# Kernel tuning notes

Measured on AMD Instinct MI355X. Metric: run time of the kernel, lower is better.

## Reference

```python
import jax, jax.numpy as jnp
import numpy as np

QLEN, MLEN, BSZ, DM, NH, DH, DI = 512, 512, 8, 1024, 16, 64, 4096
KLEN = QLEN + MLEN
EPS = 1e-5
NEG = -1e30


def layer_norm(x, g, b):
    mu = jnp.mean(x, axis=-1, keepdims=True)
    var = jnp.mean(jnp.square(x - mu), axis=-1, keepdims=True)
    return (x - mu) * jax.lax.rsqrt(var + EPS) * g + b


def rel_shift(x):
    # x: [qlen, rlen, bsz, n_head] -> Transformer-XL relative shift
    q, r, b, n = x.shape
    zp = jnp.zeros((q, 1, b, n), x.dtype)
    xp = jnp.concatenate([zp, x], axis=1).reshape(r + 1, q, b, n)
    return xp[1:].reshape(q, r, b, n)


def setup_inputs() -> dict:
    key = jax.random.key(0)
    ks = jax.random.split(key, 12)
    inp = {
        "w": jax.random.normal(ks[0], (QLEN, BSZ, DM), jnp.float32),
        "r": jax.random.normal(ks[1], (KLEN, DM), jnp.float32),
        "mems": jax.random.normal(ks[2], (MLEN, BSZ, DM), jnp.float32),
        "w_qkv": jax.random.normal(ks[3], (DM, 3 * NH * DH), jnp.float32) * 0.02,
        "w_r": jax.random.normal(ks[4], (DM, NH * DH), jnp.float32) * 0.02,
        "w_o": jax.random.normal(ks[5], (NH * DH, DM), jnp.float32) * 0.02,
        "r_w_bias": jax.random.normal(ks[6], (NH, DH), jnp.float32) * 0.02,
        "r_r_bias": jax.random.normal(ks[7], (NH, DH), jnp.float32) * 0.02,
        "ln1_g": jnp.ones((DM,), jnp.float32),
        "ln1_b": jnp.zeros((DM,), jnp.float32),
        "ff_w1": jax.random.normal(ks[8], (DM, DI), jnp.float32) * 0.02,
        "ff_b1": jnp.zeros((DI,), jnp.float32),
        "ff_w2": jax.random.normal(ks[9], (DI, DM), jnp.float32) * 0.02,
        "ff_b2": jnp.zeros((DM,), jnp.float32),
        "ln2_g": jnp.ones((DM,), jnp.float32),
        "ln2_b": jnp.zeros((DM,), jnp.float32),
    }
    # causal mask with memory: query i (global pos MLEN+i) cannot attend to j > MLEN+i
    i = jnp.arange(QLEN)[:, None]
    j = jnp.arange(KLEN)[None, :]
    inp["attn_mask"] = j > (i + MLEN)
    return inp


def reference(w, r, mems, attn_mask, w_qkv, w_r, w_o, r_w_bias, r_r_bias,
              ln1_g, ln1_b, ff_w1, ff_b1, ff_w2, ff_b2, ln2_g, ln2_b):
    qlen, bsz = w.shape[0], w.shape[1]
    scale = 1.0 / (DH ** 0.5)
    cat = jnp.concatenate([mems, w], axis=0)                 # [klen, b, d]
    klen = cat.shape[0]
    heads = cat @ w_qkv                                      # [klen, b, 3*H*D]
    hq, hk, hv = jnp.split(heads, 3, axis=-1)
    hq = hq[-qlen:].reshape(qlen, bsz, NH, DH)
    hk = hk.reshape(klen, bsz, NH, DH)
    hv = hv.reshape(klen, bsz, NH, DH)
    r_head_k = (r @ w_r).reshape(klen, NH, DH)               # [rlen, H, D]

    AC = jnp.einsum('ibnd,jbnd->ijbn', hq + r_w_bias, hk)
    BD = rel_shift(jnp.einsum('ibnd,jnd->ijbn', hq + r_r_bias, r_head_k))
    score = (AC + BD) * scale                                # [q, k, b, h]
    score = jnp.where(attn_mask[:, :, None, None], NEG, score)
    prob = jax.nn.softmax(score, axis=1)
    vec = jnp.einsum('ijbn,jbnd->ibnd', prob, hv).reshape(qlen, bsz, NH * DH)
    attn_out = vec @ w_o
    h = layer_norm(w + attn_out, ln1_g, ln1_b)               # post-LN
    ff = jax.nn.relu(h @ ff_w1 + ff_b1) @ ff_w2 + ff_b2
    return layer_norm(h + ff, ln2_g, ln2_b)
```

## Files before the change

### kernel.cpp

```cpp
#include <hip/hip_runtime.h>
#include <hip/hip_bf16.h>

#define QLEN 512
#define MLEN 512
#define KLEN 1024
#define BSZ 8
#define DM 1024
#define NH 16
#define DH 64
#define DI 4096
#define NEGF (-1e30f)
#define HM_PART ((size_t)8388608)

typedef unsigned short u16;
typedef __attribute__((ext_vector_type(8))) short short8;
typedef __attribute__((ext_vector_type(4))) short s16x4;
typedef __attribute__((ext_vector_type(4))) float f32x4;

__device__ __forceinline__ float bf2f(u16 u) {
    union { unsigned i; float f; } x; x.i = ((unsigned)u) << 16; return x.f;
}
__device__ __forceinline__ u16 f2bf(float f) {
    __hip_bfloat16 h = __float2bfloat16(f);
    return *reinterpret_cast<u16*>(&h);
}
__device__ __forceinline__ float4 ldg4(const float* p) {
    return *reinterpret_cast<const float4*>(p);
}
__device__ __forceinline__ void gload16(const void* g, void* l) {
    __builtin_amdgcn_global_load_lds(
        (const __attribute__((address_space(1))) void*)g,
        (__attribute__((address_space(3))) void*)l, 16, 0, 0);
}

__global__ __launch_bounds__(256) void cast_all(
    const float* __restrict__ mems, const float* __restrict__ w,
    const float* __restrict__ r, u16* __restrict__ catB, u16* __restrict__ rB)
{
    int idx = (blockIdx.x * 256 + threadIdx.x) * 4;
    const float* src;
    u16* dst;
    if (idx < 8388608) {
        src = (idx < 4194304) ? (mems + idx) : (w + idx - 4194304);
        dst = catB + idx;
    } else {
        int i2 = idx - 8388608;
        if (i2 >= 1048576) return;
        src = r + i2;
        dst = rB + i2;
    }
    float4 v = ldg4(src);
    u16 o[4] = { f2bf(v.x), f2bf(v.y), f2bf(v.z), f2bf(v.w) };
    *reinterpret_cast<uint2*>(dst) = *reinterpret_cast<uint2*>(o);
}

__device__ __forceinline__ void tr32(
    const float* __restrict__ W, u16* __restrict__ WT, int K, int N, int k0, int n0)
{
    __shared__ float tile[32][33];
    const int tx = threadIdx.x & 31, ty = threadIdx.x >> 5;
    #pragma unroll
    for (int j = 0; j < 4; ++j)
        tile[ty + j * 8][tx] = W[(size_t)(k0 + ty + j * 8) * N + n0 + tx];
    __syncthreads();
    #pragma unroll
    for (int j = 0; j < 4; ++j)
        WT[(size_t)(n0 + ty + j * 8) * K + k0 + tx] = f2bf(tile[tx][ty + j * 8]);
}

__global__ __launch_bounds__(256) void transpose_all(
    const float* __restrict__ w_qkv, u16* __restrict__ qkvT,
    const float* __restrict__ w_r,   u16* __restrict__ wrT,
    const float* __restrict__ w_o,   u16* __restrict__ woT,
    const float* __restrict__ ffw1,  u16* __restrict__ f1T,
    const float* __restrict__ ffw2,  u16* __restrict__ f2T)
{
    int id = blockIdx.x;
    if (id < 3072)       { int l = id;        tr32(w_qkv, qkvT, 1024, 3072, (l / 96) * 32, (l % 96) * 32); }
    else if (id < 4096)  { int l = id - 3072; tr32(w_r,   wrT,  1024, 1024, (l / 32) * 32, (l % 32) * 32); }
    else if (id < 5120)  { int l = id - 4096; tr32(w_o,   woT,  1024, 1024, (l / 32) * 32, (l % 32) * 32); }
    else if (id < 9216)  { int l = id - 5120; tr32(ffw1,  f1T,  1024, 4096, (l / 128) * 32, (l % 128) * 32); }
    else                 { int l = id - 9216; tr32(ffw2,  f2T,  4096, 1024, (l / 32) * 32, (l % 32) * 32); }
}

__global__ __launch_bounds__(256) void v_transpose(
    const u16* __restrict__ Vhm, u16* __restrict__ Vg)
{
    const int bn = blockIdx.x;
    const int kt = blockIdx.y;
    const int t = threadIdx.x;
    __shared__ u16 L[64 * 64];

    #pragma unroll
    for (int rep = 0; rep < 2; ++rep) {
        int idx = t + rep * 256;
        int key = idx >> 3, dc = (idx & 7) * 8;
        short8 v = *reinterpret_cast<const short8*>(
            &Vhm[((size_t)bn * 1024 + kt * 64 + key) * 64 + dc]);
        *reinterpret_cast<short8*>((char*)L + key * 128 + ((dc * 2) ^ ((key & 7) << 4))) = v;
    }
    __syncthreads();
    #pragma unroll
    for (int rep = 0; rep < 2; ++rep) {
        int idx = t + rep * 256;
        int d = idx >> 3, kc = (idx & 7) * 8;
        short8 o;
        #pragma unroll
        for (int e = 0; e < 8; ++e)
            o[e] = *(const short*)((char*)L + (kc + e) * 128 + ((d * 2) ^ (((kc + e) & 7) << 4)));
        *reinterpret_cast<short8*>(&Vg[((size_t)(bn * 64 + d)) * KLEN + kt * 64 + kc]) = o;
    }
}

template<bool BIAS, bool RELU, int OUT>
__global__ __launch_bounds__(256) void gemm_mfma(
    const u16* __restrict__ A, const u16* __restrict__ BT,
    const float* __restrict__ bias,
    float* __restrict__ Cf, u16* __restrict__ Cb,
    int M, int N, int K, int lda, int ldb)
{
    __shared__ u16 As[128 * 64];
    __shared__ u16 Bs[128 * 64];
    const int bm = blockIdx.y * 128, bn = blockIdx.x * 128;
    const int z = blockIdx.z;
    A  += (size_t)z * K;
    BT += (size_t)z * K;
    const size_t zoff = (size_t)z * M * N;
    const int t = threadIdx.x;
    const int w = t >> 6, l = t & 63, lg = l >> 4, lq = l & 15;
    const int wm = (w >> 1) * 64, wn = (w & 1) * 64;
    const int r8 = l >> 3, slot = l & 7;
    const int gcol = (slot * 16) ^ (r8 << 4);

    f32x4 acc[4][4];
    #pragma unroll
    for (int x = 0; x < 4; ++x)
        #pragma unroll
        for (int y = 0; y < 4; ++y)
            acc[x][y] = (f32x4){0.f, 0.f, 0.f, 0.f};

    const int swzr = (lq & 7) << 4;

    for (int k0 = 0; k0 < K; k0 += 64) {
        __syncthreads();
        #pragma unroll
        for (int it = 0; it < 4; ++it) {
            const int base_row = w * 8 + it * 32;
            gload16((const char*)A + (((size_t)(bm + base_row + r8) * lda + k0) << 1) + gcol,
                    (char*)As + base_row * 128);
            gload16((const char*)BT + (((size_t)(bn + base_row + r8) * ldb + k0) << 1) + gcol,
                    (char*)Bs + base_row * 128);
        }
        __syncthreads();
        #pragma unroll
        for (int ks = 0; ks < 2; ++ks) {
            const int cb = (ks * 64 + 16 * lg) ^ swzr;
            short8 af[4], bf_[4];
            #pragma unroll
            for (int x = 0; x < 4; ++x)
                af[x] = *reinterpret_cast<const short8*>((char*)As + (wm + 16 * x + lq) * 128 + cb);
            #pragma unroll
            for (int y = 0; y < 4; ++y)
                bf_[y] = *reinterpret_cast<const short8*>((char*)Bs + (wn + 16 * y + lq) * 128 + cb);
            #pragma unroll
            for (int x = 0; x < 4; ++x)
                #pragma unroll
                for (int y = 0; y < 4; ++y)
                    acc[x][y] = __builtin_amdgcn_mfma_f32_16x16x32_bf16(af[x], bf_[y], acc[x][y], 0, 0, 0);
        }
    }
    const int nn = ((bn + wn) >> 6) & 15;
    #pragma unroll
    for (int x = 0; x < 4; ++x) {
        #pragma unroll
        for (int y = 0; y < 4; ++y) {
            const int col = bn + wn + 16 * y + lq;
            #pragma unroll
            for (int r = 0; r < 4; ++r) {
                const int row = bm + wm + 16 * x + 4 * lg + r;
                float v = acc[x][y][r];
                if constexpr (BIAS) { if (z == 0) v += bias[col]; }
                if constexpr (RELU) v = fmaxf(v, 0.f);
                if constexpr (OUT == 0) Cf[zoff + (size_t)row * N + col] = v;
                else if constexpr (OUT == 1) Cb[zoff + (size_t)row * N + col] = f2bf(v);
                else
                    Cb[((size_t)nn * 1024 + row) * 64 + 16 * y + lq] = f2bf(v);
            }
        }
    }
}

template<bool BIAS, bool RELU, int OUT>
__global__ __launch_bounds__(512, 2) void gemm_deep(
    const u16* __restrict__ A, const u16* __restrict__ BT,
    const float* __restrict__ bias,
    float* __restrict__ Cf, u16* __restrict__ Cb,
    int M, int N, int K, int lda, int ldb)
{
    __shared__ u16 lds[3 * 24576];
    const int bm = blockIdx.y * 256, bn = blockIdx.x * 128;
    const int z = blockIdx.z;
    A  += (size_t)z * K;
    BT += (size_t)z * K;
    const size_t zoff = (size_t)z * M * N;
    const int t = threadIdx.x;
    const int w = t >> 6, l = t & 63, lg = l >> 4, lq = l & 15;
    const int wm = (w >> 1) * 64;
    const int wn = (w & 1) * 64;
    const int srow = t >> 3, slot = t & 7;
    const int gcol = (slot * 16) ^ ((srow & 7) << 4);
    const int swzr = (lq & 7) << 4;

    auto stage_tile = [&](int kt, int buf) {
        const int k0 = kt * 64;
        char* Ab = (char*)lds + buf * 49152 + w * 1024;
        char* Bb = (char*)lds + buf * 49152 + 32768 + w * 1024;
        #pragma unroll
        for (int i = 0; i < 4; ++i)
            gload16((const char*)A + (((size_t)(bm + i * 64 + srow) * lda + k0) << 1) + gcol,
                    Ab + i * 8192);
        #pragma unroll
        for (int i = 0; i < 2; ++i)
            gload16((const char*)BT + (((size_t)(bn + i * 64 + srow) * ldb + k0) << 1) + gcol,
                    Bb + i * 8192);
    };

    f32x4 acc[4][4];
    #pragma unroll
    for (int x = 0; x < 4; ++x)
        #pragma unroll
        for (int y = 0; y < 4; ++y)
            acc[x][y] = (f32x4){0.f, 0.f, 0.f, 0.f};

    const int NT = K >> 6;
    stage_tile(0, 0);
    stage_tile(1, 1);

    for (int kt = 0; kt < NT; ++kt) {
        if (kt < NT - 1) asm volatile("s_waitcnt vmcnt(6)" ::: "memory");
        else             asm volatile("s_waitcnt vmcnt(0)" ::: "memory");
        __builtin_amdgcn_s_barrier();
        __builtin_amdgcn_sched_barrier(0);
        if (kt + 2 < NT) stage_tile(kt + 2, (kt + 2) % 3);

        const char* Ab = (const char*)lds + (kt % 3) * 49152;
        const char* Bb = Ab + 32768;
        #pragma unroll
        for (int ks = 0; ks < 2; ++ks) {
            const int cb = (ks * 64 + 16 * lg) ^ swzr;
            short8 af[4], bf_[4];
            #pragma unroll
            for (int x = 0; x < 4; ++x)
                af[x] = *reinterpret_cast<const short8*>(Ab + (wm + 16 * x + lq) * 128 + cb);
            #pragma unroll
            for (int y = 0; y < 4; ++y)
                bf_[y] = *reinterpret_cast<const short8*>(Bb + (wn + 16 * y + lq) * 128 + cb);
            __builtin_amdgcn_s_setprio(1);
            #pragma unroll
            for (int x = 0; x < 4; ++x)
                #pragma unroll
                for (int y = 0; y < 4; ++y)
                    acc[x][y] = __builtin_amdgcn_mfma_f32_16x16x32_bf16(af[x], bf_[y], acc[x][y], 0, 0, 0);
            __builtin_amdgcn_s_setprio(0);
        }
    }

    #pragma unroll
    for (int x = 0; x < 4; ++x) {
        #pragma unroll
        for (int y = 0; y < 4; ++y) {
            const int col = bn + wn + 16 * y + lq;
            #pragma unroll
            for (int r = 0; r < 4; ++r) {
                const int row = bm + wm + 16 * x + 4 * lg + r;
                float v = acc[x][y][r];
                if constexpr (BIAS) { if (z == 0) v += bias[col]; }
                if constexpr (RELU) v = fmaxf(v, 0.f);
                if constexpr (OUT == 0) Cf[zoff + (size_t)row * N + col] = v;
                else Cb[zoff + (size_t)row * N + col] = f2bf(v);
            }
        }
    }
}

template<bool BIAS, bool RELU, int OUT>
__global__ __launch_bounds__(512, 2) void gemm256(
    const u16* __restrict__ A, const u16* __restrict__ BT,
    const float* __restrict__ bias, u16* __restrict__ Cb,
    int N, int K, int lda, int ldb, int nbx)
{
    __shared__ u16 lds[2 * 32768];
    int bm, bn;
    if constexpr (OUT == 2) {
        const int id = blockIdx.x;
        if (id < 64) { bm = 4096 + (id >> 2) * 256; bn = (id & 3) * 256; }
        else         { int j = id - 64; bm = (j >> 3) * 256; bn = 1024 + (j & 7) * 256; }
    } else {
        bm = (blockIdx.x / nbx) * 256; bn = (blockIdx.x % nbx) * 256;
    }
    const int t = threadIdx.x;
    const int w = t >> 6, l = t & 63, lg = l >> 4, lq = l & 15;
    const int wm = (w >> 2) * 128;
    const int wn = (w & 3) * 64;
    const int srow = t >> 3, slot = t & 7;
    const int gcol = (slot * 16) ^ ((srow & 7) << 4);
    const int swzr = (lq & 7) << 4;

    auto stage_unit = [&](int kt, char* buf, int u) {
        const int k0 = kt * 64;
        if (u < 2) {
            #pragma unroll
            for (int i = 0; i < 2; ++i) {
                int g = u * 2 + i;
                gload16((const char*)BT + (((size_t)(bn + g * 64 + srow) * ldb + k0) << 1) + gcol,
                        buf + 32768 + g * 8192 + w * 1024);
            }
        } else {
            #pragma unroll
            for (int i = 0; i < 2; ++i) {
                int g = (u - 2) + i * 2;
                gload16((const char*)A + (((size_t)(bm + g * 64 + srow) * lda + k0) << 1) + gcol,
                        buf + g * 8192 + w * 1024);
            }
        }
    };

    f32x4 acc[8][4];
    #pragma unroll
    for (int m = 0; m < 8; ++m)
        #pragma unroll
        for (int y = 0; y < 4; ++y)
            acc[m][y] = (f32x4){0.f, 0.f, 0.f, 0.f};

    const int NT = K >> 6;
    #pragma unroll
    for (int u = 0; u < 4; ++u) stage_unit(0, (char*)lds, u);

    for (int kt = 0; kt < NT; ++kt) {
        const char* Ab = (const char*)lds + (kt & 1) * 65536;
        const char* Bb = Ab + 32768;
        char* nbuf = (char*)lds + ((kt + 1) & 1) * 65536;
        const bool pf = (kt + 1 < NT);

        short8 bf_[4];
        #pragma unroll
        for (int ks = 0; ks < 2; ++ks) {
            const int cb = (ks * 64 + 16 * lg) ^ swzr;
            #pragma unroll
            for (int mh = 0; mh < 2; ++mh) {
                const int ph = ks * 2 + mh;
                if (ph == 0) {
                    asm volatile("s_waitcnt vmcnt(2)" ::: "memory");
                } else if (ph == 1) {
                    if (pf) asm volatile("s_waitcnt vmcnt(2)" ::: "memory");
                    else    asm volatile("s_waitcnt vmcnt(0)" ::: "memory");
                }
                __builtin_amdgcn_s_barrier();
                short8 af[4];
                if (mh == 0) {
                    #pragma unroll
                    for (int y = 0; y < 4; ++y)
                        bf_[y] = *reinterpret_cast<const short8*>(Bb + (wn + 16 * y + lq) * 128 + cb);
                }
                #pragma unroll
                for (int x = 0; x < 4; ++x)
                    af[x] = *reinterpret_cast<const short8*>(
                        Ab + (wm + mh * 64 + 16 * x + lq) * 128 + cb);
                if (pf) stage_unit(kt + 1, nbuf, ph);
                asm volatile("s_waitcnt lgkmcnt(0)" ::: "memory");
                __builtin_amdgcn_sched_barrier(0);
                __builtin_amdgcn_s_setprio(1);
                #pragma unroll
                for (int x = 0; x < 4; ++x)
                    #pragma unroll
                    for (int y = 0; y < 4; ++y)
                        acc[mh * 4 + x][y] = __builtin_amdgcn_mfma_f32_16x16x32_bf16(
                            af[x], bf_[y], acc[mh * 4 + x][y], 0, 0, 0);
                __builtin_amdgcn_s_setprio(0);
            }
        }
    }

    #pragma unroll
    for (int m = 0; m < 8; ++m) {
        #pragma unroll
        for (int y = 0; y < 4; ++y) {
            const int col = bn + wn + 16 * y + lq;
            #pragma unroll
            for (int r = 0; r < 4; ++r) {
                const int row = bm + wm + m * 16 + 4 * lg + r;
                float v = acc[m][y][r];
                if constexpr (BIAS) v += bias[col];
                if constexpr (RELU) v = fmaxf(v, 0.f);
                if constexpr (OUT == 2) {
                    const int part = col >> 10, nn = (col >> 6) & 15;
                    Cb[(size_t)part * HM_PART
                       + ((size_t)((row & 7) * 16 + nn) * 1024 + (row >> 3)) * 64
                       + (col & 63)] = f2bf(v);
                } else {
                    Cb[(size_t)row * N + col] = f2bf(v);
                }
            }
        }
    }
}

__global__ __launch_bounds__(512, 4) void attn_mfma(
    const u16* __restrict__ Hm,
    const u16* __restrict__ Vg,
    const u16* __restrict__ rhm,
    const float* __restrict__ rwb, const float* __restrict__ rrb,
    u16* __restrict__ vec)
{
    const int bnidx = blockIdx.x;
    const int b = bnidx >> 4;
    const int n = bnidx & 15;
    const int i0 = (3 - blockIdx.y) * 128;
    const int t = threadIdx.x;
    const int w = t >> 6;
    const int l = t & 63;
    const int lg = l >> 4, lq = l & 15;
    const int r8 = l >> 3, sl = l & 7;

    const u16* Qh = Hm;
    const u16* Kh = Hm + HM_PART;

    __shared__ u16 Ks[64 * 64];
    __shared__ u16 Vt[64 * 64];
    __shared__ u16 Rs[192 * 64];
    __shared__ u16 SbO[8 * 16 * 84];
    __shared__ u16 Ps[8 * 16 * 64];

    u16* SbW = SbO + w * 16 * 84;
    u16* PsW = Ps + w * 16 * 64;
    const int swzr = (lq & 7) << 4;
    const int stg_swz = (sl * 16) ^ (r8 << 4);

    short8 qw[2], qr[2];
    {
        const size_t qbase = ((size_t)bnidx * 1024 + MLEN + i0 + 16 * w + lq) * 64;
        #pragma unroll
        for (int ks = 0; ks < 2; ++ks) {
            short8 qv = *reinterpret_cast<const short8*>(&Qh[qbase + ks * 32 + 8 * lg]);
            short8 xw, xr;
            #pragma unroll
            for (int e = 0; e < 8; ++e) {
                float f = bf2f((u16)qv[e]);
                int d = ks * 32 + 8 * lg + e;
                xw[e] = (short)f2bf(f + rwb[n * 64 + d]);
                xr[e] = (short)f2bf(f + rrb[n * 64 + d]);
            }
            qw[ks] = xw; qr[ks] = xr;
        }
    }

    float m_run = NEGF, l_run = 0.f;
    f32x4 acc[4];
    #pragma unroll
    for (int df = 0; df < 4; ++df) acc[df] = (f32x4){0.f, 0.f, 0.f, 0.f};

    const int s0 = 112 - 16 * w;
    const int rbase = 384 - i0;
    const int ntiles = i0 / 64 + 10;

    for (int tile = 0; tile < ntiles; ++tile) {
        const int j0 = tile << 6;
        __syncthreads();
        gload16((const char*)Kh + (((size_t)bnidx * 1024 + j0 + w * 8 + r8) * 64 << 1) + stg_swz,
                (char*)Ks + w * 1024);
        gload16((const char*)Vg + ((((size_t)bnidx * 64 + w * 8 + r8) * KLEN + j0) << 1) + stg_swz,
                (char*)Vt + w * 1024);
        if (tile == 0) {
            #pragma unroll
            for (int pass = 0; pass < 3; ++pass) {
                int row = pass * 64 + w * 8 + r8;
                int o = rbase + row;
                o = o > (KLEN - 1) ? (KLEN - 1) : o;
                gload16((const char*)rhm + (((size_t)n * 1024 + o) * 64 << 1) + stg_swz,
                        (char*)Rs + pass * 8192 + w * 1024);
            }
        } else {
            const int g = tile + 2;
            int o = rbase + g * 64 + w * 8 + r8;
            o = o > (KLEN - 1) ? (KLEN - 1) : o;
            gload16((const char*)rhm + (((size_t)n * 1024 + o) * 64 << 1) + stg_swz,
                    (char*)Rs + (g % 3) * 8192 + w * 1024);
        }
        __syncthreads();

        const int bmax = i0 + 16 * w + 15 + MLEN - j0;
        if (bmax < 0) continue;

        __builtin_amdgcn_s_setprio(1);
        #pragma unroll
        for (int ff = 0; ff < 5; ++ff) {
            const int olf = s0 + 16 * ff;
            const int srowb = ((tile + (olf >> 6)) % 3) * 64 + (olf & 63);
            f32x4 d = (f32x4){0.f, 0.f, 0.f, 0.f};
            #pragma unroll
            for (int ks = 0; ks < 2; ++ks) {
                short8 a = *reinterpret_cast<const short8*>(
                    (char*)Rs + (srowb + lq) * 128 + ((ks * 64 + 16 * lg) ^ swzr));
                d = __builtin_amdgcn_mfma_f32_16x16x32_bf16(a, qr[ks], d, 0, 0, 0);
            }
            s16x4 pk;
            #pragma unroll
            for (int r = 0; r < 4; ++r) pk[r] = (short)f2bf(d[r]);
            *reinterpret_cast<s16x4*>(&SbW[lq * 84 + 16 * ff + 4 * lg]) = pk;
        }
        f32x4 dac[4];
        #pragma unroll
        for (int f = 0; f < 4; ++f) {
            f32x4 d = (f32x4){0.f, 0.f, 0.f, 0.f};
            #pragma unroll
            for (int ks = 0; ks < 2; ++ks) {
                short8 a = *reinterpret_cast<const short8*>(
                    (char*)Ks + (16 * f + lq) * 128 + ((ks * 64 + 16 * lg) ^ swzr));
                d = __builtin_amdgcn_mfma_f32_16x16x32_bf16(a, qw[ks], d, 0, 0, 0);
            }
            dac[f] = d;
        }
        __builtin_amdgcn_s_setprio(0);

        const bool fullTile = (i0 + 16 * w + MLEN - j0) >= 63;
        float sv[4][4];
        float mx = NEGF;
        if (fullTile) {
            #pragma unroll
            for (int f = 0; f < 4; ++f)
                #pragma unroll
                for (int r = 0; r < 4; ++r) {
                    int k = 16 * f + 4 * lg + r;
                    float bd = bf2f(SbW[lq * 84 + k - lq + 15]);
                    float x = (dac[f][r] + bd) * 0.125f;
                    sv[f][r] = x;
                    mx = fmaxf(mx, x);
                }
        } else {
            const int bound = i0 + 16 * w + lq + MLEN - j0;
            #pragma unroll
            for (int f = 0; f < 4; ++f)
                #pragma unroll
                for (int r = 0; r < 4; ++r) {
                    int k = 16 * f + 4 * lg + r;
                    float bd = bf2f(SbW[lq * 84 + k - lq + 15]);
                    float x = (k <= bound) ? (dac[f][r] + bd) * 0.125f : NEGF;
                    sv[f][r] = x;
                    mx = fmaxf(mx, x);
                }
        }
        mx = fmaxf(mx, __shfl_xor(mx, 16));
        mx = fmaxf(mx, __shfl_xor(mx, 32));
        const bool defer = (__all(mx <= m_run + 8.0f) != 0);
        const float m_new = defer ? m_run : fmaxf(m_run, mx);
        float ps = 0.f;
        #pragma unroll
        for (int f = 0; f < 4; ++f) {
            s16x4 pk;
            #pragma unroll
            for (int r = 0; r < 4; ++r) {
                float p = __expf(sv[f][r] - m_new);
                ps += p;
                pk[r] = (short)f2bf(p);
            }
            *reinterpret_cast<s16x4*>(
                (char*)PsW + lq * 128 + (((4 * f + lg) ^ ((lq & 7) << 1)) << 3)) = pk;
        }
        ps += __shfl_xor(ps, 16);
        ps += __shfl_xor(ps, 32);
        if (defer) {
            l_run += ps;
        } else {
            float alpha = __expf(m_run - m_new);
            l_run = l_run * alpha + ps;
            m_run = m_new;
            float alr[4];
            #pragma unroll
            for (int r = 0; r < 4; ++r) alr[r] = __shfl(alpha, 20 * lg + r);
            #pragma unroll
            for (int df = 0; df < 4; ++df)
                #pragma unroll
                for (int r = 0; r < 4; ++r) acc[df][r] *= alr[r];
        }

        __builtin_amdgcn_s_setprio(1);
        #pragma unroll
        for (int df = 0; df < 4; ++df) {
            f32x4 a = acc[df];
            #pragma unroll
            for (int ks = 0; ks < 2; ++ks) {
                short8 pa = *reinterpret_cast<const short8*>(
                    (char*)PsW + lq * 128 + ((ks * 64 + 16 * lg) ^ swzr));
                short8 vb = *reinterpret_cast<const short8*>(
                    (char*)Vt + (16 * df + lq) * 128 + ((ks * 64 + 16 * lg) ^ swzr));
                a = __builtin_amdgcn_mfma_f32_16x16x32_bf16(pa, vb, a, 0, 0, 0);
            }
            acc[df] = a;
        }
        __builtin_amdgcn_s_setprio(0);
    }

    float inv[4];
    #pragma unroll
    for (int r = 0; r < 4; ++r) inv[r] = 1.f / __shfl(l_run, 20 * lg + r);
    #pragma unroll
    for (int df = 0; df < 4; ++df) {
        #pragma unroll
        for (int r = 0; r < 4; ++r) {
            const int il = 16 * w + 4 * lg + r;
            float o = acc[df][r] * inv[r];
            vec[((size_t)((i0 + il) * BSZ + b)) * DM + n * 64 + 16 * df + lq] = f2bf(o);
        }
    }
}

template<int NRES, bool WB>
__global__ __launch_bounds__(256) void ln_res_kernel(
    const float* __restrict__ x, const float* __restrict__ res,
    const float* __restrict__ res2,
    const float* __restrict__ g, const float* __restrict__ bta,
    float* __restrict__ out, u16* __restrict__ outb)
{
    const int row = blockIdx.x;
    const int t = threadIdx.x;
    const int lane = t & 63, wv = t >> 6;
    __shared__ float red0[4], red1[4];

    float4 a = ldg4(&x[(size_t)row * DM + t * 4]);
    float4 b = ldg4(&res[(size_t)row * DM + t * 4]);
    float v0 = a.x + b.x, v1 = a.y + b.y, v2 = a.z + b.z, v3 = a.w + b.w;
    if constexpr (NRES == 2) {
        float4 c = ldg4(&res2[(size_t)row * DM + t * 4]);
        v0 += c.x; v1 += c.y; v2 += c.z; v3 += c.w;
    }
    float s = v0 + v1 + v2 + v3;
    #pragma unroll
    for (int o = 32; o; o >>= 1) s += __shfl_xor(s, o);
    if (lane == 0) red0[wv] = s;
    __syncthreads();
    float mu = (red0[0] + red0[1] + red0[2] + red0[3]) * (1.f / DM);
    float d0 = v0 - mu, d1 = v1 - mu, d2 = v2 - mu, d3 = v3 - mu;
    float q = d0*d0 + d1*d1 + d2*d2 + d3*d3;
    #pragma unroll
    for (int o = 32; o; o >>= 1) q += __shfl_xor(q, o);
    if (lane == 0) red1[wv] = q;
    __syncthreads();
    float var = (red1[0] + red1[1] + red1[2] + red1[3]) * (1.f / DM);
    float rs = rsqrtf(var + 1e-5f);
    float4 gv = ldg4(&g[t * 4]);
    float4 bv = ldg4(&bta[t * 4]);
    float o0 = d0 * rs * gv.x + bv.x;
    float o1 = d1 * rs * gv.y + bv.y;
    float o2 = d2 * rs * gv.z + bv.z;
    float o3 = d3 * rs * gv.w + bv.w;
    float4 o4 = make_float4(o0, o1, o2, o3);
    *reinterpret_cast<float4*>(&out[(size_t)row * DM + t * 4]) = o4;
    if constexpr (WB) {
        u16 ob[4] = { f2bf(o0), f2bf(o1), f2bf(o2), f2bf(o3) };
        *reinterpret_cast<uint2*>(&outb[(size_t)row * DM + t * 4]) = *reinterpret_cast<uint2*>(ob);
    }
}

extern "C" void kernel_launch(void* const* d_in, const int* in_sizes, int n_in,
                              void* d_out, int out_size, void* d_ws, size_t ws_size,
                              hipStream_t stream) {
    const float* w     = (const float*)d_in[0];
    const float* r     = (const float*)d_in[1];
    const float* mems  = (const float*)d_in[2];
    const float* w_qkv = (const float*)d_in[3];
    const float* w_r   = (const float*)d_in[4];
    const float* w_o   = (const float*)d_in[5];
    const float* rwb   = (const float*)d_in[6];
    const float* rrb   = (const float*)d_in[7];
    const float* ln1g  = (const float*)d_in[8];
    const float* ln1b  = (const float*)d_in[9];
    const float* ffw1  = (const float*)d_in[10];
    const float* ffb1  = (const float*)d_in[11];
    const float* ffw2  = (const float*)d_in[12];
    const float* ffb2  = (const float*)d_in[13];
    const float* ln2g  = (const float*)d_in[14];
    const float* ln2b  = (const float*)d_in[15];
    (void)in_sizes; (void)n_in; (void)out_size; (void)ws_size;

    char* p = (char*)d_ws;
    auto alloc = [&](size_t bytes) { char* q = p; p += (bytes + 255) & ~(size_t)255; return q; };
    u16* catB   = (u16*)alloc((size_t)8192 * 1024 * 2);
    u16* rB     = (u16*)alloc((size_t)1024 * 1024 * 2);
    u16* qkvT   = (u16*)alloc((size_t)3072 * 1024 * 2);
    u16* wrT    = (u16*)alloc((size_t)1024 * 1024 * 2);
    u16* woT    = (u16*)alloc((size_t)1024 * 1024 * 2);
    u16* f1T    = (u16*)alloc((size_t)4096 * 1024 * 2);
    u16* f2T    = (u16*)alloc((size_t)1024 * 4096 * 2);
    u16* headsHm= (u16*)alloc((size_t)3 * HM_PART * 2);
    u16* rhkHm  = (u16*)alloc((size_t)1024 * 1024 * 2);
    u16* vec    = (u16*)alloc((size_t)4096 * 1024 * 2);
    u16* hB     = (u16*)alloc((size_t)4096 * 1024 * 2);
    u16* ff1    = (u16*)alloc((size_t)4096 * 4096 * 2);
    float* hF   = (float*)alloc((size_t)4096 * 1024 * 4);

    u16* Vg = catB;
    float* attn_out = (float*)ff1;
    float* ff2 = (float*)headsHm;
    float* outp = (float*)d_out;

    cast_all<<<9216, 256, 0, stream>>>(mems, w, r, catB, rB);
    transpose_all<<<13312, 256, 0, stream>>>(w_qkv, qkvT, w_r, wrT, w_o, woT,
                                             ffw1, f1T, ffw2, f2T);

    gemm256<false, false, 2><<<320, 512, 0, stream>>>(
        catB, qkvT, nullptr, headsHm, 3072, 1024, 1024, 1024, 0);
    v_transpose<<<dim3(128, 16), 256, 0, stream>>>(headsHm + 2 * HM_PART, Vg);
    gemm_mfma<false, false, 3><<<dim3(8, 8), 256, 0, stream>>>(
        rB, wrT, nullptr, nullptr, rhkHm, 1024, 1024, 1024, 1024, 1024);
    attn_mfma<<<dim3(BSZ * NH, QLEN / 128), 512, 0, stream>>>(
        headsHm, Vg, rhkHm, rwb, rrb, vec);
    gemm_mfma<false, false, 0><<<dim3(8, 32, 2), 256, 0, stream>>>(
        vec, woT, nullptr, attn_out, nullptr, 4096, 1024, 512, 1024, 1024);
    ln_res_kernel<2, true><<<4096, 256, 0, stream>>>(
        w, attn_out, attn_out + (size_t)4096 * 1024, ln1g, ln1b, hF, hB);
    gemm256<true, true, 1><<<256, 512, 0, stream>>>(
        hB, f1T, ffb1, ff1, 4096, 1024, 1024, 1024, 16);
    gemm_deep<true, false, 0><<<dim3(8, 16, 2), 512, 0, stream>>>(
        ff1, f2T, ffb2, ff2, nullptr, 4096, 1024, 2048, 4096, 4096);
    ln_res_kernel<2, false><<<4096, 256, 0, stream>>>(
        hF, ff2, ff2 + (size_t)4096 * 1024, ln2g, ln2b, outp, nullptr);
}
```

Baseline: 304.2 us.

## Use 4-way split-K gemm256 with bf16 partials for output and FFN2 GEMMs

```diff
diff --git a/kernel.cpp b/kernel.cpp
--- a/kernel.cpp
+++ b/kernel.cpp
@@ -122,10 +122,6 @@
     __shared__ u16 As[128 * 64];
     __shared__ u16 Bs[128 * 64];
     const int bm = blockIdx.y * 128, bn = blockIdx.x * 128;
-    const int z = blockIdx.z;
-    A  += (size_t)z * K;
-    BT += (size_t)z * K;
-    const size_t zoff = (size_t)z * M * N;
     const int t = threadIdx.x;
     const int w = t >> 6, l = t & 63, lg = l >> 4, lq = l & 15;
     const int wm = (w >> 1) * 64, wn = (w & 1) * 64;
@@ -179,105 +175,12 @@
             for (int r = 0; r < 4; ++r) {
                 const int row = bm + wm + 16 * x + 4 * lg + r;
                 float v = acc[x][y][r];
-                if constexpr (BIAS) { if (z == 0) v += bias[col]; }
+                if constexpr (BIAS) v += bias[col];
                 if constexpr (RELU) v = fmaxf(v, 0.f);
-                if constexpr (OUT == 0) Cf[zoff + (size_t)row * N + col] = v;
-                else if constexpr (OUT == 1) Cb[zoff + (size_t)row * N + col] = f2bf(v);
+                if constexpr (OUT == 0) Cf[(size_t)row * N + col] = v;
+                else if constexpr (OUT == 1) Cb[(size_t)row * N + col] = f2bf(v);
                 else
                     Cb[((size_t)nn * 1024 + row) * 64 + 16 * y + lq] = f2bf(v);
-            }
-        }
-    }
-}
-
-template<bool BIAS, bool RELU, int OUT>
-__global__ __launch_bounds__(512, 2) void gemm_deep(
-    const u16* __restrict__ A, const u16* __restrict__ BT,
-    const float* __restrict__ bias,
-    float* __restrict__ Cf, u16* __restrict__ Cb,
-    int M, int N, int K, int lda, int ldb)
-{
-    __shared__ u16 lds[3 * 24576];
-    const int bm = blockIdx.y * 256, bn = blockIdx.x * 128;
-    const int z = blockIdx.z;
-    A  += (size_t)z * K;
-    BT += (size_t)z * K;
-    const size_t zoff = (size_t)z * M * N;
-    const int t = threadIdx.x;
-    const int w = t >> 6, l = t & 63, lg = l >> 4, lq = l & 15;
-    const int wm = (w >> 1) * 64;
-    const int wn = (w & 1) * 64;
-    const int srow = t >> 3, slot = t & 7;
-    const int gcol = (slot * 16) ^ ((srow & 7) << 4);
-    const int swzr = (lq & 7) << 4;
-
-    auto stage_tile = [&](int kt, int buf) {
-        const int k0 = kt * 64;
-        char* Ab = (char*)lds + buf * 49152 + w * 1024;
-        char* Bb = (char*)lds + buf * 49152 + 32768 + w * 1024;
-        #pragma unroll
-        for (int i = 0; i < 4; ++i)
-            gload16((const char*)A + (((size_t)(bm + i * 64 + srow) * lda + k0) << 1) + gcol,
-                    Ab + i * 8192);
-        #pragma unroll
-        for (int i = 0; i < 2; ++i)
-            gload16((const char*)BT + (((size_t)(bn + i * 64 + srow) * ldb + k0) << 1) + gcol,
-                    Bb + i * 8192);
-    };
-
-    f32x4 acc[4][4];
-    #pragma unroll
-    for (int x = 0; x < 4; ++x)
-        #pragma unroll
-        for (int y = 0; y < 4; ++y)
-            acc[x][y] = (f32x4){0.f, 0.f, 0.f, 0.f};
-
-    const int NT = K >> 6;
-    stage_tile(0, 0);
-    stage_tile(1, 1);
-
-    for (int kt = 0; kt < NT; ++kt) {
-        if (kt < NT - 1) asm volatile("s_waitcnt vmcnt(6)" ::: "memory");
-        else             asm volatile("s_waitcnt vmcnt(0)" ::: "memory");
-        __builtin_amdgcn_s_barrier();
-        __builtin_amdgcn_sched_barrier(0);
-        if (kt + 2 < NT) stage_tile(kt + 2, (kt + 2) % 3);
-
-        const char* Ab = (const char*)lds + (kt % 3) * 49152;
-        const char* Bb = Ab + 32768;
-        #pragma unroll
-        for (int ks = 0; ks < 2; ++ks) {
-            const int cb = (ks * 64 + 16 * lg) ^ swzr;
-            short8 af[4], bf_[4];
-            #pragma unroll
-            for (int x = 0; x < 4; ++x)
-                af[x] = *reinterpret_cast<const short8*>(Ab + (wm + 16 * x + lq) * 128 + cb);
-            #pragma unroll
-            for (int y = 0; y < 4; ++y)
-                bf_[y] = *reinterpret_cast<const short8*>(Bb + (wn + 16 * y + lq) * 128 + cb);
-            __builtin_amdgcn_s_setprio(1);
-            #pragma unroll
-            for (int x = 0; x < 4; ++x)
-                #pragma unroll
-                for (int y = 0; y < 4; ++y)
-                    acc[x][y] = __builtin_amdgcn_mfma_f32_16x16x32_bf16(af[x], bf_[y], acc[x][y], 0, 0, 0);
-            __builtin_amdgcn_s_setprio(0);
-        }
-    }
-
-    #pragma unroll
-    for (int x = 0; x < 4; ++x) {
-        #pragma unroll
-        for (int y = 0; y < 4; ++y) {
-            const int col = bn + wn + 16 * y + lq;
-            #pragma unroll
-            for (int r = 0; r < 4; ++r) {
-                const int row = bm + wm + 16 * x + 4 * lg + r;
-                float v = acc[x][y][r];
-                if constexpr (BIAS) { if (z == 0) v += bias[col]; }
-                if constexpr (RELU) v = fmaxf(v, 0.f);
-                if constexpr (OUT == 0) Cf[zoff + (size_t)row * N + col] = v;
-                else Cb[zoff + (size_t)row * N + col] = f2bf(v);
             }
         }
     }
@@ -287,7 +190,7 @@
 __global__ __launch_bounds__(512, 2) void gemm256(
     const u16* __restrict__ A, const u16* __restrict__ BT,
     const float* __restrict__ bias, u16* __restrict__ Cb,
-    int N, int K, int lda, int ldb, int nbx)
+    int N, int K, int lda, int ldb, int nbx, size_t zstride)
 {
     __shared__ u16 lds[2 * 32768];
     int bm, bn;
@@ -298,6 +201,10 @@
     } else {
         bm = (blockIdx.x / nbx) * 256; bn = (blockIdx.x % nbx) * 256;
     }
+    const int z = blockIdx.z;
+    A  += (size_t)z * K;
+    BT += (size_t)z * K;
+    Cb += (size_t)z * zstride;
     const int t = threadIdx.x;
     const int w = t >> 6, l = t & 63, lg = l >> 4, lq = l & 15;
     const int wm = (w >> 2) * 128;
@@ -390,7 +297,7 @@
             for (int r = 0; r < 4; ++r) {
                 const int row = bm + wm + m * 16 + 4 * lg + r;
                 float v = acc[m][y][r];
-                if constexpr (BIAS) v += bias[col];
+                if constexpr (BIAS) { if (z == 0) v += bias[col]; }
                 if constexpr (RELU) v = fmaxf(v, 0.f);
                 if constexpr (OUT == 2) {
                     const int part = col >> 10, nn = (col >> 6) & 15;
@@ -447,8 +354,8 @@
             for (int e = 0; e < 8; ++e) {
                 float f = bf2f((u16)qv[e]);
                 int d = ks * 32 + 8 * lg + e;
-                xw[e] = (short)f2bf(f + rwb[n * 64 + d]);
-                xr[e] = (short)f2bf(f + rrb[n * 64 + d]);
+                xw[e] = (short)f2bf((f + rwb[n * 64 + d]) * 0.125f);
+                xr[e] = (short)f2bf((f + rrb[n * 64 + d]) * 0.125f);
             }
             qw[ks] = xw; qr[ks] = xr;
         }
@@ -531,8 +438,7 @@
                 #pragma unroll
                 for (int r = 0; r < 4; ++r) {
                     int k = 16 * f + 4 * lg + r;
-                    float bd = bf2f(SbW[lq * 84 + k - lq + 15]);
-                    float x = (dac[f][r] + bd) * 0.125f;
+                    float x = dac[f][r] + bf2f(SbW[lq * 84 + k - lq + 15]);
                     sv[f][r] = x;
                     mx = fmaxf(mx, x);
                 }
@@ -543,8 +449,8 @@
                 #pragma unroll
                 for (int r = 0; r < 4; ++r) {
                     int k = 16 * f + 4 * lg + r;
-                    float bd = bf2f(SbW[lq * 84 + k - lq + 15]);
-                    float x = (k <= bound) ? (dac[f][r] + bd) * 0.125f : NEGF;
+                    float x = (k <= bound)
+                        ? dac[f][r] + bf2f(SbW[lq * 84 + k - lq + 15]) : NEGF;
                     sv[f][r] = x;
                     mx = fmaxf(mx, x);
                 }
@@ -616,8 +522,9 @@
 
 template<int NRES, bool WB>
 __global__ __launch_bounds__(256) void ln_res_kernel(
-    const float* __restrict__ x, const float* __restrict__ res,
-    const float* __restrict__ res2,
+    const float* __restrict__ x,
+    const u16* __restrict__ r0, const u16* __restrict__ r1,
+    const u16* __restrict__ r2, const u16* __restrict__ r3,
     const float* __restrict__ g, const float* __restrict__ bta,
     float* __restrict__ out, u16* __restrict__ outb)
 {
@@ -626,12 +533,17 @@
     const int lane = t & 63, wv = t >> 6;
     __shared__ float red0[4], red1[4];
 
-    float4 a = ldg4(&x[(size_t)row * DM + t * 4]);
-    float4 b = ldg4(&res[(size_t)row * DM + t * 4]);
-    float v0 = a.x + b.x, v1 = a.y + b.y, v2 = a.z + b.z, v3 = a.w + b.w;
-    if constexpr (NRES == 2) {
-        float4 c = ldg4(&res2[(size_t)row * DM + t * 4]);
-        v0 += c.x; v1 += c.y; v2 += c.z; v3 += c.w;
+    const size_t base = (size_t)row * DM + t * 4;
+    float4 a = ldg4(&x[base]);
+    float v0 = a.x, v1 = a.y, v2 = a.z, v3 = a.w;
+    const u16* rs[4] = { r0, r1, r2, r3 };
+    #pragma unroll
+    for (int s = 0; s < NRES; ++s) {
+        uint2 u = *reinterpret_cast<const uint2*>(&rs[s][base]);
+        v0 += bf2f((u16)(u.x & 0xffff));
+        v1 += bf2f((u16)(u.x >> 16));
+        v2 += bf2f((u16)(u.y & 0xffff));
+        v3 += bf2f((u16)(u.y >> 16));
     }
     float s = v0 + v1 + v2 + v3;
     #pragma unroll
@@ -646,18 +558,18 @@
     if (lane == 0) red1[wv] = q;
     __syncthreads();
     float var = (red1[0] + red1[1] + red1[2] + red1[3]) * (1.f / DM);
-    float rs = rsqrtf(var + 1e-5f);
+    float rsq = rsqrtf(var + 1e-5f);
     float4 gv = ldg4(&g[t * 4]);
     float4 bv = ldg4(&bta[t * 4]);
-    float o0 = d0 * rs * gv.x + bv.x;
-    float o1 = d1 * rs * gv.y + bv.y;
-    float o2 = d2 * rs * gv.z + bv.z;
-    float o3 = d3 * rs * gv.w + bv.w;
+    float o0 = d0 * rsq * gv.x + bv.x;
+    float o1 = d1 * rsq * gv.y + bv.y;
+    float o2 = d2 * rsq * gv.z + bv.z;
+    float o3 = d3 * rsq * gv.w + bv.w;
     float4 o4 = make_float4(o0, o1, o2, o3);
-    *reinterpret_cast<float4*>(&out[(size_t)row * DM + t * 4]) = o4;
+    *reinterpret_cast<float4*>(&out[base]) = o4;
     if constexpr (WB) {
         u16 ob[4] = { f2bf(o0), f2bf(o1), f2bf(o2), f2bf(o3) };
-        *reinterpret_cast<uint2*>(&outb[(size_t)row * DM + t * 4]) = *reinterpret_cast<uint2*>(ob);
+        *reinterpret_cast<uint2*>(&outb[base]) = *reinterpret_cast<uint2*>(ob);
     }
 }
 
@@ -699,8 +611,9 @@
     float* hF   = (float*)alloc((size_t)4096 * 1024 * 4);
 
     u16* Vg = catB;
-    float* attn_out = (float*)ff1;
-    float* ff2 = (float*)headsHm;
+    u16* aoP = ff1;
+    u16* f2P = headsHm;
+    const size_t PSTR = (size_t)4096 * 1024;
     float* outp = (float*)d_out;
 
     cast_all<<<9216, 256, 0, stream>>>(mems, w, r, catB, rB);
@@ -708,20 +621,20 @@
                                              ffw1, f1T, ffw2, f2T);
 
     gemm256<false, false, 2><<<320, 512, 0, stream>>>(
-        catB, qkvT, nullptr, headsHm, 3072, 1024, 1024, 1024, 0);
+        catB, qkvT, nullptr, headsHm, 3072, 1024, 1024, 1024, 0, 0);
     v_transpose<<<dim3(128, 16), 256, 0, stream>>>(headsHm + 2 * HM_PART, Vg);
     gemm_mfma<false, false, 3><<<dim3(8, 8), 256, 0, stream>>>(
         rB, wrT, nullptr, nullptr, rhkHm, 1024, 1024, 1024, 1024, 1024);
     attn_mfma<<<dim3(BSZ * NH, QLEN / 128), 512, 0, stream>>>(
         headsHm, Vg, rhkHm, rwb, rrb, vec);
-    gemm_mfma<false, false, 0><<<dim3(8, 32, 2), 256, 0, stream>>>(
-        vec, woT, nullptr, attn_out, nullptr, 4096, 1024, 512, 1024, 1024);
-    ln_res_kernel<2, true><<<4096, 256, 0, stream>>>(
-        w, attn_out, attn_out + (size_t)4096 * 1024, ln1g, ln1b, hF, hB);
-    gemm256<true, true, 1><<<256, 512, 0, stream>>>(
-        hB, f1T, ffb1, ff1, 4096, 1024, 1024, 1024, 16);
-    gemm_deep<true, false, 0><<<dim3(8, 16, 2), 512, 0, stream>>>(
-        ff1, f2T, ffb2, ff2, nullptr, 4096, 1024, 2048, 4096, 4096);
-    ln_res_kernel<2, false><<<4096, 256, 0, stream>>>(
-        hF, ff2, ff2 + (size_t)4096 * 1024, ln2g, ln2b, outp, nullptr);
-}
+    gemm256<false, false, 1><<<dim3(64, 1, 4), 512, 0, stream>>>(
+        vec, woT, nullptr, aoP, 1024, 256, 1024, 1024, 4, PSTR);
+    ln_res_kernel<4, true><<<4096, 256, 0, stream>>>(
+        w, aoP, aoP + PSTR, aoP + 2 * PSTR, aoP + 3 * PSTR, ln1g, ln1b, hF, hB);
+    gemm256<true, true, 1><<<dim3(256, 1, 1), 512, 0, stream>>>(
+        hB, f1T, ffb1, ff1, 4096, 1024, 1024, 1024, 16, 0);
+    gemm256<true, false, 1><<<dim3(64, 1, 4), 512, 0, stream>>>(
+        ff1, f2T, ffb2, f2P, 1024, 1024, 4096, 4096, 4, PSTR);
+    ln_res_kernel<4, false><<<4096, 256, 0, stream>>>(
+        hF, f2P, f2P + PSTR, f2P + 2 * PSTR, f2P + 3 * PSTR, ln2g, ln2b, outp, nullptr);
+}
```

Result: slower. 311.3 us (+2.3%).

## Register-prefetch next K/V/R tiles and fold softmax scale into Q

Applied to the files above, without the earlier changes.

```diff
diff --git a/kernel.cpp b/kernel.cpp
--- a/kernel.cpp
+++ b/kernel.cpp
@@ -16,6 +16,7 @@
 typedef __attribute__((ext_vector_type(8))) short short8;
 typedef __attribute__((ext_vector_type(4))) short s16x4;
 typedef __attribute__((ext_vector_type(4))) float f32x4;
+typedef __attribute__((ext_vector_type(4))) unsigned int u32x4;
 
 __device__ __forceinline__ float bf2f(u16 u) {
     union { unsigned i; float f; } x; x.i = ((unsigned)u) << 16; return x.f;
@@ -435,6 +436,21 @@
     u16* PsW = Ps + w * 16 * 64;
     const int swzr = (lq & 7) << 4;
     const int stg_swz = (sl * 16) ^ (r8 << 4);
+    const int lofs = l * 16;
+    const int rbase = 384 - i0;
+    const int ntiles = i0 / 64 + 10;
+
+    auto kSrc = [&](int tile) {
+        return (const char*)Kh + (((size_t)bnidx * 1024 + (tile << 6) + w * 8 + r8) * 64 << 1) + stg_swz;
+    };
+    auto vSrc = [&](int tile) {
+        return (const char*)Vg + ((((size_t)bnidx * 64 + w * 8 + r8) * KLEN + (tile << 6)) << 1) + stg_swz;
+    };
+    auto rSrc = [&](int g) {
+        int o = rbase + g * 64 + w * 8 + r8;
+        o = o > (KLEN - 1) ? (KLEN - 1) : o;
+        return (const char*)rhm + (((size_t)n * 1024 + o) * 64 << 1) + stg_swz;
+    };
 
     short8 qw[2], qr[2];
     {
@@ -447,8 +463,8 @@
             for (int e = 0; e < 8; ++e) {
                 float f = bf2f((u16)qv[e]);
                 int d = ks * 32 + 8 * lg + e;
-                xw[e] = (short)f2bf(f + rwb[n * 64 + d]);
-                xr[e] = (short)f2bf(f + rrb[n * 64 + d]);
+                xw[e] = (short)f2bf((f + rwb[n * 64 + d]) * 0.125f);
+                xr[e] = (short)f2bf((f + rrb[n * 64 + d]) * 0.125f);
             }
             qw[ks] = xw; qr[ks] = xr;
         }
@@ -460,33 +476,34 @@
     for (int df = 0; df < 4; ++df) acc[df] = (f32x4){0.f, 0.f, 0.f, 0.f};
 
     const int s0 = 112 - 16 * w;
-    const int rbase = 384 - i0;
-    const int ntiles = i0 / 64 + 10;
+
+    u32x4 kreg = *reinterpret_cast<const u32x4*>(kSrc(0));
+    u32x4 vreg = *reinterpret_cast<const u32x4*>(vSrc(0));
+    u32x4 rr0  = *reinterpret_cast<const u32x4*>(rSrc(0));
+    u32x4 rr1  = *reinterpret_cast<const u32x4*>(rSrc(1));
+    u32x4 rr2  = *reinterpret_cast<const u32x4*>(rSrc(2));
 
     for (int tile = 0; tile < ntiles; ++tile) {
         const int j0 = tile << 6;
-        __syncthreads();
-        gload16((const char*)Kh + (((size_t)bnidx * 1024 + j0 + w * 8 + r8) * 64 << 1) + stg_swz,
-                (char*)Ks + w * 1024);
-        gload16((const char*)Vg + ((((size_t)bnidx * 64 + w * 8 + r8) * KLEN + j0) << 1) + stg_swz,
-                (char*)Vt + w * 1024);
+        __builtin_amdgcn_s_barrier();
+        __builtin_amdgcn_sched_barrier(0);
+        *reinterpret_cast<u32x4*>((char*)Ks + w * 1024 + lofs) = kreg;
+        *reinterpret_cast<u32x4*>((char*)Vt + w * 1024 + lofs) = vreg;
         if (tile == 0) {
-            #pragma unroll
-            for (int pass = 0; pass < 3; ++pass) {
-                int row = pass * 64 + w * 8 + r8;
-                int o = rbase + row;
-                o = o > (KLEN - 1) ? (KLEN - 1) : o;
-                gload16((const char*)rhm + (((size_t)n * 1024 + o) * 64 << 1) + stg_swz,
-                        (char*)Rs + pass * 8192 + w * 1024);
-            }
+            *reinterpret_cast<u32x4*>((char*)Rs + 0 * 8192 + w * 1024 + lofs) = rr0;
+            *reinterpret_cast<u32x4*>((char*)Rs + 1 * 8192 + w * 1024 + lofs) = rr1;
+            *reinterpret_cast<u32x4*>((char*)Rs + 2 * 8192 + w * 1024 + lofs) = rr2;
         } else {
-            const int g = tile + 2;
-            int o = rbase + g * 64 + w * 8 + r8;
-            o = o > (KLEN - 1) ? (KLEN - 1) : o;
-            gload16((const char*)rhm + (((size_t)n * 1024 + o) * 64 << 1) + stg_swz,
-                    (char*)Rs + (g % 3) * 8192 + w * 1024);
-        }
-        __syncthreads();
+            *reinterpret_cast<u32x4*>((char*)Rs + ((tile + 2) % 3) * 8192 + w * 1024 + lofs) = rr0;
+        }
+        if (tile + 1 < ntiles) {
+            kreg = *reinterpret_cast<const u32x4*>(kSrc(tile + 1));
+            vreg = *reinterpret_cast<const u32x4*>(vSrc(tile + 1));
+            rr0  = *reinterpret_cast<const u32x4*>(rSrc(tile + 3));
+        }
+        asm volatile("s_waitcnt lgkmcnt(0)" ::: "memory");
+        __builtin_amdgcn_s_barrier();
+        __builtin_amdgcn_sched_barrier(0);
 
         const int bmax = i0 + 16 * w + 15 + MLEN - j0;
         if (bmax < 0) continue;
@@ -531,8 +548,7 @@
                 #pragma unroll
                 for (int r = 0; r < 4; ++r) {
                     int k = 16 * f + 4 * lg + r;
-                    float bd = bf2f(SbW[lq * 84 + k - lq + 15]);
-                    float x = (dac[f][r] + bd) * 0.125f;
+                    float x = dac[f][r] + bf2f(SbW[lq * 84 + k - lq + 15]);
                     sv[f][r] = x;
                     mx = fmaxf(mx, x);
                 }
@@ -543,8 +559,8 @@
                 #pragma unroll
                 for (int r = 0; r < 4; ++r) {
                     int k = 16 * f + 4 * lg + r;
-                    float bd = bf2f(SbW[lq * 84 + k - lq + 15]);
-                    float x = (k <= bound) ? (dac[f][r] + bd) * 0.125f : NEGF;
+                    float x = (k <= bound)
+                        ? dac[f][r] + bf2f(SbW[lq * 84 + k - lq + 15]) : NEGF;
                     sv[f][r] = x;
                     mx = fmaxf(mx, x);
                 }
```

Result: no change. 301.7 us (-0.8%).
